# Kernel optimization log

Hardware: AMD Instinct MI355X
Metric: run time of the kernel (lower is better)

The kernel has to match this reference:

```python
import jax, jax.numpy as jnp
import numpy as np

HIDDEN = 2048
N_HEADS = 16
HEAD_DIM = HIDDEN // N_HEADS
FF_DIM = 5632  # int(2*4*2048/3)=5461 rounded up to multiple of 256
ROPE_THETA = 500000.0
NORM_EPS = 1e-5
B, S = 2, 2048


def apply_rope(x, positions, inv_freq):
    # x: [B,S,H,D], positions: [B,S], inv_freq: [D/2]
    angles = positions.astype(inv_freq.dtype)[..., None] * inv_freq[None, None, :]
    cos = jnp.cos(angles)[:, :, None, :]
    sin = jnp.sin(angles)[:, :, None, :]
    x_pair = x.reshape(*x.shape[:-1], x.shape[-1] // 2, 2)
    x0, x1 = x_pair[..., 0], x_pair[..., 1]
    out = jnp.stack([x0 * cos - x1 * sin, x1 * cos + x0 * sin], axis=-1)
    return out.reshape(x.shape).astype(x.dtype)


def rmsnorm(x, scale, eps=NORM_EPS):
    var = jnp.mean(jnp.square(x), axis=-1, keepdims=True)
    return (x * jax.lax.rsqrt(var + eps)) * scale


def setup_inputs() -> dict:
    key = jax.random.key(0)
    ks = jax.random.split(key, 12)
    sd = 1.0 / np.sqrt(HIDDEN)
    sdf = 1.0 / np.sqrt(FF_DIM)
    x = jax.random.normal(ks[0], (B, S, HIDDEN), dtype=jnp.float32)
    positions = jnp.tile(jnp.arange(S, dtype=jnp.int32)[None, :], (B, 1))
    mask = jnp.tril(jnp.ones((S, S), dtype=jnp.bool_))[None].repeat(B, axis=0)
    return {
        "x": x,
        "positions": positions,
        "mask": mask,
        "wq": jax.random.normal(ks[1], (HIDDEN, HIDDEN), jnp.float32) * sd,
        "wk": jax.random.normal(ks[2], (HIDDEN, HIDDEN), jnp.float32) * sd,
        "wv": jax.random.normal(ks[3], (HIDDEN, HIDDEN), jnp.float32) * sd,
        "wo": jax.random.normal(ks[4], (HIDDEN, HIDDEN), jnp.float32) * sd,
        "attn_scale": jnp.ones((HIDDEN,), jnp.float32),
        "ffn_scale": jnp.ones((HIDDEN,), jnp.float32),
        "w1": jax.random.normal(ks[5], (HIDDEN, FF_DIM), jnp.float32) * sd,
        "w3": jax.random.normal(ks[6], (HIDDEN, FF_DIM), jnp.float32) * sd,
        "w2": jax.random.normal(ks[7], (FF_DIM, HIDDEN), jnp.float32) * sdf,
    }


def reference(x, positions, mask, wq, wk, wv, wo, attn_scale, ffn_scale, w1, w3, w2):
    Bx = x.shape[0]
    inv_freq = 1.0 / ROPE_THETA ** (jnp.arange(0, HEAD_DIM, 2, dtype=jnp.float32) / HEAD_DIM)
    x_norm = rmsnorm(x, attn_scale)
    q = apply_rope((x_norm @ wq).reshape(Bx, -1, N_HEADS, HEAD_DIM), positions, inv_freq)
    k = apply_rope((x_norm @ wk).reshape(Bx, -1, N_HEADS, HEAD_DIM), positions, inv_freq)
    v = (x_norm @ wv).reshape(Bx, -1, N_HEADS, HEAD_DIM)
    scale = 1.0 / jnp.sqrt(jnp.float32(HEAD_DIM)).astype(q.dtype)
    # [B,H,S,S]
    attn_weights = jnp.einsum("bqhd,bkhd->bhqk", q, k) * scale
    big_neg = jnp.finfo(q.dtype).min
    attn_weights = jnp.where(mask[:, None, :, :], attn_weights, big_neg)
    attn_weights = jax.nn.softmax(attn_weights, axis=-1)
    attn_out = jnp.einsum("bhqk,bkhd->bqhd", attn_weights, v).reshape(Bx, -1, HIDDEN)
    h = x + attn_out @ wo
    ff = rmsnorm(h, ffn_scale)
    return h + (jax.nn.silu(ff @ w1) * (ff @ w3)) @ w2
```

## Files before the change

kernel.cpp:

```cpp
#include <hip/hip_runtime.h>

#define HID 2048
#define SEQ 2048
#define NB 2
#define NHD 16
#define HD 128
#define FF 5632
#define MROWS 4096

typedef __bf16 bf16x8 __attribute__((ext_vector_type(8)));
typedef float f32x4 __attribute__((ext_vector_type(4)));
typedef unsigned short u16;
typedef unsigned int u32;
typedef unsigned long long u64;

__device__ __forceinline__ u16 f2bf(float f) {
  u32 u = __float_as_uint(f);
  u += 0x7fffu + ((u >> 16) & 1u);
  return (u16)(u >> 16);
}
__device__ __forceinline__ float bf2f(u16 h) {
  return __uint_as_float(((u32)h) << 16);
}
__device__ __forceinline__ void gld16(const void* g, void* l) {
  __builtin_amdgcn_global_load_lds((__attribute__((address_space(1))) void*)g,
                                   (__attribute__((address_space(3))) void*)l, 16, 0, 0);
}

__global__ __launch_bounds__(256) void rmsnorm_k(const float* __restrict__ x,
                                                 const float* __restrict__ sc,
                                                 u16* __restrict__ out) {
  __shared__ float red[4];
  const int row = blockIdx.x, t = threadIdx.x;
  const float4* xr = (const float4*)(x + (size_t)row * HID);
  float4 a = xr[t], b = xr[t + 256];
  float ss = a.x*a.x + a.y*a.y + a.z*a.z + a.w*a.w
           + b.x*b.x + b.y*b.y + b.z*b.z + b.w*b.w;
#pragma unroll
  for (int o = 1; o < 64; o <<= 1) ss += __shfl_xor(ss, o);
  if ((t & 63) == 0) red[t >> 6] = ss;
  __syncthreads();
  float tot = red[0] + red[1] + red[2] + red[3];
  float r = rsqrtf(tot * (1.0f / HID) + 1e-5f);
  const float4* scp = (const float4*)sc;
  float4 s0 = scp[t], s1 = scp[t + 256];
  u32 p0 = (u32)f2bf(a.x*r*s0.x) | ((u32)f2bf(a.y*r*s0.y) << 16);
  u32 p1 = (u32)f2bf(a.z*r*s0.z) | ((u32)f2bf(a.w*r*s0.w) << 16);
  u32 p2 = (u32)f2bf(b.x*r*s1.x) | ((u32)f2bf(b.y*r*s1.y) << 16);
  u32 p3 = (u32)f2bf(b.z*r*s1.z) | ((u32)f2bf(b.w*r*s1.w) << 16);
  u32* op = (u32*)(out + (size_t)row * HID);
  op[t*2] = p0; op[t*2+1] = p1;
  op[512 + t*2] = p2; op[512 + t*2 + 1] = p3;
}

__global__ __launch_bounds__(256) void transpose_cvt_k(const float* __restrict__ W,
                                                       u16* __restrict__ Wt,
                                                       int R, int C) {
  __shared__ float tile[32][33];
  const int tx = threadIdx.x & 31, ty = threadIdx.x >> 5;
  const int bc = blockIdx.x * 32, br = blockIdx.y * 32;
#pragma unroll
  for (int i = 0; i < 4; ++i)
    tile[ty + i*8][tx] = W[(size_t)(br + ty + i*8) * C + bc + tx];
  __syncthreads();
#pragma unroll
  for (int i = 0; i < 4; ++i)
    Wt[(size_t)(bc + ty + i*8) * R + br + tx] = f2bf(tile[tx][ty + i*8]);
}

__global__ __launch_bounds__(256) void rope_k(u16* __restrict__ qk, const int* __restrict__ pos) {
  const u32 i = blockIdx.x * 256 + threadIdx.x;
  const int d2 = i & 63;
  const int s = (i >> 6) & 2047;
  const int bh = i >> 17;
  const int b = bh >> 4;
  const float p = (float)pos[(size_t)b * SEQ + s];
  const float ang = p * exp2f(-(float)d2 * 0.2958057589f);
  float sv, cv;
  sincosf(ang, &sv, &cv);
  u32* ptr = (u32*)(qk + ((size_t)bh * SEQ + s) * HD) + d2;
  u32 u = *ptr;
  float x0 = bf2f((u16)(u & 0xffff)), x1 = bf2f((u16)(u >> 16));
  float o0 = x0 * cv - x1 * sv;
  float o1 = x1 * cv + x0 * sv;
  *ptr = (u32)f2bf(o0) | ((u32)f2bf(o1) << 16);
}

template <int EPI>
__global__ __launch_bounds__(256, 2) void gemm_k(const u16* __restrict__ A,
                                                 const u16* __restrict__ Bt,
                                                 int N, int K,
                                                 const float* addsrc,
                                                 const u16* mulsrc,
                                                 void* outp) {
  __shared__ __align__(16) u16 As[128 * 32];
  __shared__ __align__(16) u16 Bs[128 * 32];
  const int tid = threadIdx.x, lane = tid & 63, wid = tid >> 6;
  const int lr = lane & 15, lg = lane >> 4;
  const int wr = wid >> 1, wc = wid & 1;
  const int mt = blockIdx.y * 128, nt = blockIdx.x * 128;

  const f32x4 fz = {0.f, 0.f, 0.f, 0.f};
  f32x4 acc[4][4];
#pragma unroll
  for (int i = 0; i < 4; ++i)
#pragma unroll
    for (int j = 0; j < 4; ++j) acc[i][j] = fz;

  const int r0 = wid * 32 + (lane >> 2);
  const int c0 = (lane & 3) * 8;
  u16* ldsA0 = As + wid * 1024;
  u16* ldsA1 = As + wid * 1024 + 512;
  u16* ldsB0 = Bs + wid * 1024;
  u16* ldsB1 = Bs + wid * 1024 + 512;
  const u16* Abase = A + (size_t)mt * K;
  const u16* Bbase = Bt + (size_t)nt * K;

  for (int kt = 0; kt < K; kt += 32) {
    gld16(Abase + (size_t)r0 * K + kt + c0, ldsA0);
    gld16(Abase + (size_t)(r0 + 16) * K + kt + c0, ldsA1);
    gld16(Bbase + (size_t)r0 * K + kt + c0, ldsB0);
    gld16(Bbase + (size_t)(r0 + 16) * K + kt + c0, ldsB1);
    __syncthreads();
    bf16x8 af[4], bfr[4];
#pragma unroll
    for (int mi = 0; mi < 4; ++mi)
      af[mi] = *(const bf16x8*)(As + (wr * 64 + mi * 16 + lr) * 32 + lg * 8);
#pragma unroll
    for (int ni = 0; ni < 4; ++ni)
      bfr[ni] = *(const bf16x8*)(Bs + (wc * 64 + ni * 16 + lr) * 32 + lg * 8);
#pragma unroll
    for (int mi = 0; mi < 4; ++mi)
#pragma unroll
      for (int ni = 0; ni < 4; ++ni)
        acc[mi][ni] = __builtin_amdgcn_mfma_f32_16x16x32_bf16(af[mi], bfr[ni], acc[mi][ni], 0, 0, 0);
    __syncthreads();
  }

#pragma unroll
  for (int mi = 0; mi < 4; ++mi) {
#pragma unroll
    for (int ni = 0; ni < 4; ++ni) {
      const int gr0 = mt + wr * 64 + mi * 16 + lg * 4;
      const int gc = nt + wc * 64 + ni * 16 + lr;
      f32x4 v = acc[mi][ni];
      if (EPI == 5) {
        const int b = gr0 >> 11, s = gr0 & 2047, hh = gc >> 7, d = gc & 127;
        u64 pk = (u64)f2bf(v[0])
               | ((u64)f2bf(v[1]) << 16)
               | ((u64)f2bf(v[2]) << 32)
               | ((u64)f2bf(v[3]) << 48);
        *(u64*)((u16*)outp + ((((size_t)(b * NHD + hh)) * HD + d) << 11) + s) = pk;
      } else {
#pragma unroll
        for (int r = 0; r < 4; ++r) {
          const int gr = gr0 + r;
          const float val = v[r];
          if (EPI == 1) {
            const int b = gr >> 11, s = gr & 2047, hh = gc >> 7, d = gc & 127;
            ((u16*)outp)[((((size_t)(b * NHD + hh)) * SEQ + s) << 7) + d] = f2bf(val);
          } else if (EPI == 2) {
            const size_t o = (size_t)gr * N + gc;
            ((float*)outp)[o] = addsrc[o] + val;
          } else if (EPI == 3) {
            const size_t o = (size_t)gr * N + gc;
            ((u16*)outp)[o] = f2bf(val / (1.f + __expf(-val)));
          } else if (EPI == 4) {
            const size_t o = (size_t)gr * N + gc;
            ((u16*)outp)[o] = f2bf(bf2f(mulsrc[o]) * val);
          }
        }
      }
    }
  }
}

#define ATT_SW(row) (((row) & 7) << 4)

__device__ __forceinline__ void att_stage(const u16* __restrict__ Kp,
                                          const u16* __restrict__ Vp,
                                          int kt, char* kb, char* vb,
                                          int tid, int wid) {
#pragma unroll
  for (int j = 0; j < 4; ++j) {
    const int c = j * 256 + tid;
    const int row = c >> 4;
    const int scb = ((c & 15) << 4) ^ ATT_SW(row);
    gld16(Kp + (size_t)(kt + row) * HD + (scb >> 1), kb + j * 4096 + wid * 1024);
  }
#pragma unroll
  for (int j = 0; j < 4; ++j) {
    const int c = j * 256 + tid;
    const int row = c >> 3;
    const int scb = ((c & 7) << 4) ^ ATT_SW(row);
    gld16(Vp + (size_t)row * SEQ + kt + (scb >> 1), vb + j * 4096 + wid * 1024);
  }
}

__global__ __launch_bounds__(256, 2) void attn_k(const u16* __restrict__ Q,
                                                 const u16* __restrict__ Kg,
                                                 const u16* __restrict__ Vtg,
                                                 u16* __restrict__ out) {
  __shared__ __align__(16) char Kb[2][16384];
  __shared__ __align__(16) char Vb[2][16384];
  __shared__ __align__(16) u16 Pl[4][16 * 72];
  const int tid = threadIdx.x, lane = tid & 63, wid = tid >> 6;
  const int lr = lane & 15, lg = lane >> 4;
  int wg = blockIdx.x;
  wg = (wg & 7) * 64 + (wg >> 3);
  const int bh = wg >> 4, pr = wg & 15;
  const size_t bhoff = (size_t)bh * SEQ * HD;
  const u16* Qp = Q + bhoff;
  const u16* Kp = Kg + bhoff;
  const u16* Vp = Vtg + bhoff;
  const int bb = bh >> 4, hh = bh & 15;
  u16* Pw = Pl[wid];
  const int sw = ATT_SW(lr);
  const float scale = 0.08838834764831845f;
  const f32x4 fz = {0.f, 0.f, 0.f, 0.f};

  for (int side = 0; side < 2; ++side) {
    const int qt = side ? (31 - pr) : pr;
    const int qrow0 = qt * 64 + wid * 16;

    bf16x8 qf[4];
#pragma unroll
    for (int t = 0; t < 4; ++t)
      qf[t] = *(const bf16x8*)(Qp + (size_t)(qrow0 + lr) * HD + t * 32 + lg * 8);

    f32x4 o[8];
#pragma unroll
    for (int i = 0; i < 8; ++i) o[i] = fz;
    float mrun[4] = {-1e30f, -1e30f, -1e30f, -1e30f};
    float lrun[4] = {0.f, 0.f, 0.f, 0.f};

    const int kend = qt * 64 + 64;
    int cur = 0;
    att_stage(Kp, Vp, 0, Kb[0], Vb[0], tid, wid);
    __syncthreads();

    for (int kt = 0; kt < kend; kt += 64) {
      if (kt + 64 < kend)
        att_stage(Kp, Vp, kt + 64, Kb[cur ^ 1], Vb[cur ^ 1], tid, wid);
      const char* kbuf = Kb[cur];
      const char* vbuf = Vb[cur];

      f32x4 sc[4];
#pragma unroll
      for (int nh = 0; nh < 4; ++nh) {
        f32x4 s = fz;
#pragma unroll
        for (int t = 0; t < 4; ++t) {
          bf16x8 kf = *(const bf16x8*)(kbuf + (nh * 16 + lr) * 256 + ((t * 64 + lg * 16) ^ sw));
          s = __builtin_amdgcn_mfma_f32_16x16x32_bf16(qf[t], kf, s, 0, 0, 0);
        }
        sc[nh] = s;
      }

      float pv[4][4], alpha[4];
#pragma unroll
      for (int r = 0; r < 4; ++r) {
        const int qrow = qrow0 + lg * 4 + r;
        float s0 = sc[0][r] * scale;
        float s1 = sc[1][r] * scale;
        float s2 = sc[2][r] * scale;
        float s3 = sc[3][r] * scale;
        if (kt + lr > qrow)      s0 = -1e30f;
        if (kt + 16 + lr > qrow) s1 = -1e30f;
        if (kt + 32 + lr > qrow) s2 = -1e30f;
        if (kt + 48 + lr > qrow) s3 = -1e30f;
        float mx = fmaxf(fmaxf(s0, s1), fmaxf(s2, s3));
        mx = fmaxf(mx, __shfl_xor(mx, 1));
        mx = fmaxf(mx, __shfl_xor(mx, 2));
        mx = fmaxf(mx, __shfl_xor(mx, 4));
        mx = fmaxf(mx, __shfl_xor(mx, 8));
        const float mn = fmaxf(mrun[r], mx);
        const float p0 = __expf(s0 - mn), p1 = __expf(s1 - mn);
        const float p2 = __expf(s2 - mn), p3 = __expf(s3 - mn);
        float ts = p0 + p1 + p2 + p3;
        ts += __shfl_xor(ts, 1);
        ts += __shfl_xor(ts, 2);
        ts += __shfl_xor(ts, 4);
        ts += __shfl_xor(ts, 8);
        const float al = __expf(mrun[r] - mn);
        alpha[r] = al;
        lrun[r] = lrun[r] * al + ts;
        mrun[r] = mn;
        pv[0][r] = p0; pv[1][r] = p1; pv[2][r] = p2; pv[3][r] = p3;
      }
#pragma unroll
      for (int i = 0; i < 8; ++i) {
        o[i][0] *= alpha[0]; o[i][1] *= alpha[1];
        o[i][2] *= alpha[2]; o[i][3] *= alpha[3];
      }

#pragma unroll
      for (int nh = 0; nh < 4; ++nh)
#pragma unroll
        for (int r = 0; r < 4; ++r)
          Pw[(lg * 4 + r) * 72 + nh * 16 + lr] = f2bf(pv[nh][r]);
      asm volatile("s_waitcnt lgkmcnt(0)\n" ::: "memory");
      const bf16x8 pf0 = *(const bf16x8*)(Pw + lr * 72 + lg * 8);
      const bf16x8 pf1 = *(const bf16x8*)(Pw + lr * 72 + 32 + lg * 8);

#pragma unroll
      for (int nt = 0; nt < 8; ++nt) {
        const char* vr = vbuf + (nt * 16 + lr) * 128;
        bf16x8 v0 = *(const bf16x8*)(vr + ((lg * 16) ^ sw));
        bf16x8 v1 = *(const bf16x8*)(vr + ((64 + lg * 16) ^ sw));
        o[nt] = __builtin_amdgcn_mfma_f32_16x16x32_bf16(pf0, v0, o[nt], 0, 0, 0);
        o[nt] = __builtin_amdgcn_mfma_f32_16x16x32_bf16(pf1, v1, o[nt], 0, 0, 0);
      }
      __syncthreads();
      cur ^= 1;
    }

#pragma unroll
    for (int r = 0; r < 4; ++r) {
      const int q = qrow0 + lg * 4 + r;
      const float inv = 1.f / lrun[r];
      u16* op = out + ((size_t)(bb * SEQ + q)) * HID + hh * HD + lr;
#pragma unroll
      for (int nt = 0; nt < 8; ++nt)
        op[nt * 16] = f2bf(o[nt][r] * inv);
    }
  }
}

extern "C" void kernel_launch(void* const* d_in, const int* in_sizes, int n_in,
                              void* d_out, int out_size, void* d_ws, size_t ws_size,
                              hipStream_t stream) {
  (void)in_sizes; (void)n_in; (void)out_size; (void)ws_size;
  const float* x   = (const float*)d_in[0];
  const int*   pos = (const int*)d_in[1];
  const float* wq  = (const float*)d_in[3];
  const float* wk  = (const float*)d_in[4];
  const float* wv  = (const float*)d_in[5];
  const float* wo  = (const float*)d_in[6];
  const float* asc = (const float*)d_in[7];
  const float* fsc = (const float*)d_in[8];
  const float* w1  = (const float*)d_in[9];
  const float* w3  = (const float*)d_in[10];
  const float* w2  = (const float*)d_in[11];
  float* out = (float*)d_out;

  char* ws = (char*)d_ws;
  u16* qb = (u16*)ws; ws += (size_t)MROWS * HID * 2;
  u16* kb = (u16*)ws; ws += (size_t)MROWS * HID * 2;
  u16* vb = (u16*)ws; ws += (size_t)MROWS * HID * 2;
  u16* xb = (u16*)ws; ws += (size_t)MROWS * HID * 2;
  u16* gb = (u16*)ws; ws += (size_t)MROWS * FF * 2;
  u16* wb = (u16*)ws; ws += (size_t)FF * HID * 2;

  dim3 b256(256);

  rmsnorm_k<<<MROWS, b256, 0, stream>>>(x, asc, xb);

  transpose_cvt_k<<<dim3(HID/32, HID/32), b256, 0, stream>>>(wq, wb, HID, HID);
  gemm_k<1><<<dim3(HID/128, MROWS/128), b256, 0, stream>>>(xb, wb, HID, HID, nullptr, nullptr, qb);
  transpose_cvt_k<<<dim3(HID/32, HID/32), b256, 0, stream>>>(wk, wb, HID, HID);
  gemm_k<1><<<dim3(HID/128, MROWS/128), b256, 0, stream>>>(xb, wb, HID, HID, nullptr, nullptr, kb);
  transpose_cvt_k<<<dim3(HID/32, HID/32), b256, 0, stream>>>(wv, wb, HID, HID);
  gemm_k<5><<<dim3(HID/128, MROWS/128), b256, 0, stream>>>(xb, wb, HID, HID, nullptr, nullptr, vb);

  rope_k<<<(NB*NHD*SEQ*(HD/2))/256, b256, 0, stream>>>(qb, pos);
  rope_k<<<(NB*NHD*SEQ*(HD/2))/256, b256, 0, stream>>>(kb, pos);

  attn_k<<<dim3(512), b256, 0, stream>>>(qb, kb, vb, xb);

  transpose_cvt_k<<<dim3(HID/32, HID/32), b256, 0, stream>>>(wo, wb, HID, HID);
  gemm_k<2><<<dim3(HID/128, MROWS/128), b256, 0, stream>>>(xb, wb, HID, HID, x, nullptr, out);

  rmsnorm_k<<<MROWS, b256, 0, stream>>>(out, fsc, xb);

  transpose_cvt_k<<<dim3(FF/32, HID/32), b256, 0, stream>>>(w1, wb, HID, FF);
  gemm_k<3><<<dim3(FF/128, MROWS/128), b256, 0, stream>>>(xb, wb, FF, HID, nullptr, nullptr, gb);
  transpose_cvt_k<<<dim3(FF/32, HID/32), b256, 0, stream>>>(w3, wb, HID, FF);
  gemm_k<4><<<dim3(FF/128, MROWS/128), b256, 0, stream>>>(xb, wb, FF, HID, nullptr, gb, gb);
  transpose_cvt_k<<<dim3(HID/32, FF/32), b256, 0, stream>>>(w2, wb, FF, HID);
  gemm_k<2><<<dim3(HID/128, MROWS/128), b256, 0, stream>>>(gb, wb, HID, FF, out, nullptr, out);
}
```

Measured before the change: 1.003 ms.

## Replace GEMM with 256x256 double-buffered pipelined kernel and fuse QKV projection

```diff
diff --git a/kernel.cpp b/kernel.cpp
--- a/kernel.cpp
+++ b/kernel.cpp
@@ -86,80 +86,139 @@
   *ptr = (u32)f2bf(o0) | ((u32)f2bf(o1) << 16);
 }
 
+#define VMW(N) asm volatile("s_waitcnt vmcnt(" #N ")" ::: "memory")
+#define BARR() do { __builtin_amdgcn_s_barrier(); __builtin_amdgcn_sched_barrier(0); } while (0)
+
+#define STAGE_A(NB, H) do { \
+  gld16(ap + (size_t)((H)*128) * K,      &Ab[NB][(H)*8192 + wid*512]); \
+  gld16(ap + (size_t)((H)*128 + 64) * K, &Ab[NB][(H)*8192 + 4096 + wid*512]); \
+} while (0)
+#define STAGE_B(NB, H) do { \
+  gld16(bp + (size_t)((H)*128) * K,      &Bb[NB][(H)*8192 + wid*512]); \
+  gld16(bp + (size_t)((H)*128 + 64) * K, &Bb[NB][(H)*8192 + 4096 + wid*512]); \
+} while (0)
+#define READ_A(BF, AH) do { \
+  const char* pa_ = (const char*)Ab[BF] + (AH)*16384 + arow; \
+  av[0][0] = *(const bf16x8*)(pa_ + 0*4096 + ck0); av[0][1] = *(const bf16x8*)(pa_ + 0*4096 + ck1); \
+  av[1][0] = *(const bf16x8*)(pa_ + 1*4096 + ck0); av[1][1] = *(const bf16x8*)(pa_ + 1*4096 + ck1); \
+  av[2][0] = *(const bf16x8*)(pa_ + 2*4096 + ck0); av[2][1] = *(const bf16x8*)(pa_ + 2*4096 + ck1); \
+  av[3][0] = *(const bf16x8*)(pa_ + 3*4096 + ck0); av[3][1] = *(const bf16x8*)(pa_ + 3*4096 + ck1); \
+} while (0)
+#define READ_B(BF, BH) do { \
+  const char* pb_ = (const char*)Bb[BF] + (BH)*16384 + brow; \
+  bv[(BH)*2+0][0] = *(const bf16x8*)(pb_ + 0*8192 + ck0); bv[(BH)*2+0][1] = *(const bf16x8*)(pb_ + 0*8192 + ck1); \
+  bv[(BH)*2+1][0] = *(const bf16x8*)(pb_ + 1*8192 + ck0); bv[(BH)*2+1][1] = *(const bf16x8*)(pb_ + 1*8192 + ck1); \
+} while (0)
+#define MMAQ(AH, BH) do { \
+  __builtin_amdgcn_s_setprio(1); \
+  _Pragma("unroll") \
+  for (int kk_ = 0; kk_ < 2; ++kk_) \
+    _Pragma("unroll") \
+    for (int m_ = 0; m_ < 4; ++m_) \
+      _Pragma("unroll") \
+      for (int n_ = 0; n_ < 2; ++n_) \
+        acc[(AH)*4+m_][(BH)*2+n_] = __builtin_amdgcn_mfma_f32_16x16x32_bf16( \
+            av[m_][kk_], bv[(BH)*2+n_][kk_], acc[(AH)*4+m_][(BH)*2+n_], 0, 0, 0); \
+  __builtin_amdgcn_s_setprio(0); \
+} while (0)
+
 template <int EPI>
-__global__ __launch_bounds__(256, 2) void gemm_k(const u16* __restrict__ A,
-                                                 const u16* __restrict__ Bt,
-                                                 int N, int K,
-                                                 const float* addsrc,
-                                                 const u16* mulsrc,
-                                                 void* outp) {
-  __shared__ __align__(16) u16 As[128 * 32];
-  __shared__ __align__(16) u16 Bs[128 * 32];
+__global__ __launch_bounds__(512, 2) void gemm256_k(const u16* __restrict__ A,
+                                                    const u16* __restrict__ Bt,
+                                                    int N, int K,
+                                                    const float* __restrict__ addsrc,
+                                                    const u16* __restrict__ mulsrc,
+                                                    void* __restrict__ outp) {
+  __shared__ __align__(16) u16 Ab[2][16384];
+  __shared__ __align__(16) u16 Bb[2][16384];
   const int tid = threadIdx.x, lane = tid & 63, wid = tid >> 6;
   const int lr = lane & 15, lg = lane >> 4;
-  const int wr = wid >> 1, wc = wid & 1;
-  const int mt = blockIdx.y * 128, nt = blockIdx.x * 128;
+  const int wr = wid >> 2, wc = wid & 3;
+
+  const int gx = gridDim.x;
+  int bid = blockIdx.y * gx + blockIdx.x;
+  const int q8 = (gx * gridDim.y) >> 3;
+  bid = (bid & 7) * q8 + (bid >> 3);
+  const int mt = (bid / gx) * 256, nt = (bid % gx) * 256;
 
   const f32x4 fz = {0.f, 0.f, 0.f, 0.f};
-  f32x4 acc[4][4];
-#pragma unroll
-  for (int i = 0; i < 4; ++i)
+  f32x4 acc[8][4];
+#pragma unroll
+  for (int i = 0; i < 8; ++i)
 #pragma unroll
     for (int j = 0; j < 4; ++j) acc[i][j] = fz;
 
-  const int r0 = wid * 32 + (lane >> 2);
-  const int c0 = (lane & 3) * 8;
-  u16* ldsA0 = As + wid * 1024;
-  u16* ldsA1 = As + wid * 1024 + 512;
-  u16* ldsB0 = Bs + wid * 1024;
-  u16* ldsB1 = Bs + wid * 1024 + 512;
-  const u16* Abase = A + (size_t)mt * K;
-  const u16* Bbase = Bt + (size_t)nt * K;
-
-  for (int kt = 0; kt < K; kt += 32) {
-    gld16(Abase + (size_t)r0 * K + kt + c0, ldsA0);
-    gld16(Abase + (size_t)(r0 + 16) * K + kt + c0, ldsA1);
-    gld16(Bbase + (size_t)r0 * K + kt + c0, ldsB0);
-    gld16(Bbase + (size_t)(r0 + 16) * K + kt + c0, ldsB1);
-    __syncthreads();
-    bf16x8 af[4], bfr[4];
-#pragma unroll
-    for (int mi = 0; mi < 4; ++mi)
-      af[mi] = *(const bf16x8*)(As + (wr * 64 + mi * 16 + lr) * 32 + lg * 8);
-#pragma unroll
-    for (int ni = 0; ni < 4; ++ni)
-      bfr[ni] = *(const bf16x8*)(Bs + (wc * 64 + ni * 16 + lr) * 32 + lg * 8);
-#pragma unroll
-    for (int mi = 0; mi < 4; ++mi)
-#pragma unroll
-      for (int ni = 0; ni < 4; ++ni)
-        acc[mi][ni] = __builtin_amdgcn_mfma_f32_16x16x32_bf16(af[mi], bfr[ni], acc[mi][ni], 0, 0, 0);
-    __syncthreads();
+  const int srow = tid >> 3;
+  const int scol = ((((tid & 7) * 16) ^ (((srow >> 2) & 1) << 5)) >> 1);
+  const u16* ap = A  + (size_t)(mt + srow) * K + scol;
+  const u16* bp = Bt + (size_t)(nt + srow) * K + scol;
+
+  const int arow = (wr * 16 + lr) * 128;
+  const int brow = (wc * 16 + lr) * 128;
+  const int swl = ((lr >> 2) & 1) << 5;
+  const int ck0 = (lg * 16) ^ swl;
+  const int ck1 = (64 + lg * 16) ^ swl;
+
+  bf16x8 av[4][2], bv[4][2];
+
+  STAGE_A(0, 0); STAGE_B(0, 0); STAGE_B(0, 1); STAGE_A(0, 1);
+  ap += 64; bp += 64;
+
+  const int ntk = K >> 6;
+  int buf = 0;
+  for (int t = 0; t < ntk - 1; ++t) {
+    const int nb = buf ^ 1;
+    STAGE_A(nb, 0);  VMW(6); BARR();
+    READ_A(buf, 0);  READ_B(buf, 0);  MMAQ(0, 0);
+    STAGE_B(nb, 0);  VMW(6); BARR();
+    READ_B(buf, 1);  MMAQ(0, 1);
+    STAGE_B(nb, 1);  VMW(6); BARR();
+    READ_A(buf, 1);  MMAQ(1, 1);
+    STAGE_A(nb, 1);
+    MMAQ(1, 0);
+    ap += 64; bp += 64;
+    buf = nb;
   }
-
-#pragma unroll
-  for (int mi = 0; mi < 4; ++mi) {
+  VMW(4); BARR();
+  READ_A(buf, 0); READ_B(buf, 0); MMAQ(0, 0);
+  VMW(2); BARR();
+  READ_B(buf, 1); MMAQ(0, 1);
+  VMW(0); BARR();
+  READ_A(buf, 1); MMAQ(1, 1);
+  MMAQ(1, 0);
+
+#pragma unroll
+  for (int mi = 0; mi < 8; ++mi) {
 #pragma unroll
     for (int ni = 0; ni < 4; ++ni) {
-      const int gr0 = mt + wr * 64 + mi * 16 + lg * 4;
-      const int gc = nt + wc * 64 + ni * 16 + lr;
+      const int gr0 = mt + mi * 32 + wr * 16 + lg * 4;
+      const int gc = nt + ni * 64 + wc * 16 + lr;
       f32x4 v = acc[mi][ni];
-      if (EPI == 5) {
-        const int b = gr0 >> 11, s = gr0 & 2047, hh = gc >> 7, d = gc & 127;
-        u64 pk = (u64)f2bf(v[0])
-               | ((u64)f2bf(v[1]) << 16)
-               | ((u64)f2bf(v[2]) << 32)
-               | ((u64)f2bf(v[3]) << 48);
-        *(u64*)((u16*)outp + ((((size_t)(b * NHD + hh)) * HD + d) << 11) + s) = pk;
+      if (EPI == 1) {
+        const int which = gc >> 11;
+        const int c2 = gc & 2047;
+        const int hh = c2 >> 7, d = c2 & 127;
+        if (which < 2) {
+          u16* dst = (u16*)outp + (size_t)which * ((size_t)MROWS * HID);
+#pragma unroll
+          for (int r = 0; r < 4; ++r) {
+            const int gr = gr0 + r;
+            const int b = gr >> 11, s = gr & 2047;
+            dst[((((size_t)(b * NHD + hh)) * SEQ + s) << 7) + d] = f2bf(v[r]);
+          }
+        } else {
+          u16* dst = (u16*)outp + (size_t)2 * ((size_t)MROWS * HID);
+          const int b = gr0 >> 11, s0 = gr0 & 2047;
+          u64 pk = (u64)f2bf(v[0]) | ((u64)f2bf(v[1]) << 16)
+                 | ((u64)f2bf(v[2]) << 32) | ((u64)f2bf(v[3]) << 48);
+          *(u64*)(dst + ((((size_t)(b * NHD + hh)) * HD + d) << 11) + s0) = pk;
+        }
       } else {
 #pragma unroll
         for (int r = 0; r < 4; ++r) {
           const int gr = gr0 + r;
           const float val = v[r];
-          if (EPI == 1) {
-            const int b = gr >> 11, s = gr & 2047, hh = gc >> 7, d = gc & 127;
-            ((u16*)outp)[((((size_t)(b * NHD + hh)) * SEQ + s) << 7) + d] = f2bf(val);
-          } else if (EPI == 2) {
+          if (EPI == 2) {
             const size_t o = (size_t)gr * N + gc;
             ((float*)outp)[o] = addsrc[o] + val;
           } else if (EPI == 3) {
@@ -245,7 +304,7 @@
       const char* kbuf = Kb[cur];
       const char* vbuf = Vb[cur];
 
-      f32x4 sc[4];
+      f32x4 sc2[4];
 #pragma unroll
       for (int nh = 0; nh < 4; ++nh) {
         f32x4 s = fz;
@@ -254,17 +313,17 @@
           bf16x8 kf = *(const bf16x8*)(kbuf + (nh * 16 + lr) * 256 + ((t * 64 + lg * 16) ^ sw));
           s = __builtin_amdgcn_mfma_f32_16x16x32_bf16(qf[t], kf, s, 0, 0, 0);
         }
-        sc[nh] = s;
+        sc2[nh] = s;
       }
 
       float pv[4][4], alpha[4];
 #pragma unroll
       for (int r = 0; r < 4; ++r) {
         const int qrow = qrow0 + lg * 4 + r;
-        float s0 = sc[0][r] * scale;
-        float s1 = sc[1][r] * scale;
-        float s2 = sc[2][r] * scale;
-        float s3 = sc[3][r] * scale;
+        float s0 = sc2[0][r] * scale;
+        float s1 = sc2[1][r] * scale;
+        float s2 = sc2[2][r] * scale;
+        float s3 = sc2[3][r] * scale;
         if (kt + lr > qrow)      s0 = -1e30f;
         if (kt + 16 + lr > qrow) s1 = -1e30f;
         if (kt + 32 + lr > qrow) s2 = -1e30f;
@@ -304,12 +363,12 @@
       const bf16x8 pf1 = *(const bf16x8*)(Pw + lr * 72 + 32 + lg * 8);
 
 #pragma unroll
-      for (int nt = 0; nt < 8; ++nt) {
-        const char* vr = vbuf + (nt * 16 + lr) * 128;
+      for (int nt2 = 0; nt2 < 8; ++nt2) {
+        const char* vr = vbuf + (nt2 * 16 + lr) * 128;
         bf16x8 v0 = *(const bf16x8*)(vr + ((lg * 16) ^ sw));
         bf16x8 v1 = *(const bf16x8*)(vr + ((64 + lg * 16) ^ sw));
-        o[nt] = __builtin_amdgcn_mfma_f32_16x16x32_bf16(pf0, v0, o[nt], 0, 0, 0);
-        o[nt] = __builtin_amdgcn_mfma_f32_16x16x32_bf16(pf1, v1, o[nt], 0, 0, 0);
+        o[nt2] = __builtin_amdgcn_mfma_f32_16x16x32_bf16(pf0, v0, o[nt2], 0, 0, 0);
+        o[nt2] = __builtin_amdgcn_mfma_f32_16x16x32_bf16(pf1, v1, o[nt2], 0, 0, 0);
       }
       __syncthreads();
       cur ^= 1;
@@ -321,8 +380,8 @@
       const float inv = 1.f / lrun[r];
       u16* op = out + ((size_t)(bb * SEQ + q)) * HID + hh * HD + lr;
 #pragma unroll
-      for (int nt = 0; nt < 8; ++nt)
-        op[nt * 16] = f2bf(o[nt][r] * inv);
+      for (int nt2 = 0; nt2 < 8; ++nt2)
+        op[nt2 * 16] = f2bf(o[nt2][r] * inv);
     }
   }
 }
@@ -351,17 +410,16 @@
   u16* xb = (u16*)ws; ws += (size_t)MROWS * HID * 2;
   u16* gb = (u16*)ws; ws += (size_t)MROWS * FF * 2;
   u16* wb = (u16*)ws; ws += (size_t)FF * HID * 2;
-
-  dim3 b256(256);
+  u16* wqkvT = gb;
+
+  dim3 b256(256), b512(512);
 
   rmsnorm_k<<<MROWS, b256, 0, stream>>>(x, asc, xb);
 
-  transpose_cvt_k<<<dim3(HID/32, HID/32), b256, 0, stream>>>(wq, wb, HID, HID);
-  gemm_k<1><<<dim3(HID/128, MROWS/128), b256, 0, stream>>>(xb, wb, HID, HID, nullptr, nullptr, qb);
-  transpose_cvt_k<<<dim3(HID/32, HID/32), b256, 0, stream>>>(wk, wb, HID, HID);
-  gemm_k<1><<<dim3(HID/128, MROWS/128), b256, 0, stream>>>(xb, wb, HID, HID, nullptr, nullptr, kb);
-  transpose_cvt_k<<<dim3(HID/32, HID/32), b256, 0, stream>>>(wv, wb, HID, HID);
-  gemm_k<5><<<dim3(HID/128, MROWS/128), b256, 0, stream>>>(xb, wb, HID, HID, nullptr, nullptr, vb);
+  transpose_cvt_k<<<dim3(HID/32, HID/32), b256, 0, stream>>>(wq, wqkvT, HID, HID);
+  transpose_cvt_k<<<dim3(HID/32, HID/32), b256, 0, stream>>>(wk, wqkvT + (size_t)HID*HID, HID, HID);
+  transpose_cvt_k<<<dim3(HID/32, HID/32), b256, 0, stream>>>(wv, wqkvT + (size_t)2*HID*HID, HID, HID);
+  gemm256_k<1><<<dim3(3*HID/256, MROWS/256), b512, 0, stream>>>(xb, wqkvT, 3*HID, HID, nullptr, nullptr, qb);
 
   rope_k<<<(NB*NHD*SEQ*(HD/2))/256, b256, 0, stream>>>(qb, pos);
   rope_k<<<(NB*NHD*SEQ*(HD/2))/256, b256, 0, stream>>>(kb, pos);
@@ -369,14 +427,14 @@
   attn_k<<<dim3(512), b256, 0, stream>>>(qb, kb, vb, xb);
 
   transpose_cvt_k<<<dim3(HID/32, HID/32), b256, 0, stream>>>(wo, wb, HID, HID);
-  gemm_k<2><<<dim3(HID/128, MROWS/128), b256, 0, stream>>>(xb, wb, HID, HID, x, nullptr, out);
+  gemm256_k<2><<<dim3(HID/256, MROWS/256), b512, 0, stream>>>(xb, wb, HID, HID, x, nullptr, out);
 
   rmsnorm_k<<<MROWS, b256, 0, stream>>>(out, fsc, xb);
 
   transpose_cvt_k<<<dim3(FF/32, HID/32), b256, 0, stream>>>(w1, wb, HID, FF);
-  gemm_k<3><<<dim3(FF/128, MROWS/128), b256, 0, stream>>>(xb, wb, FF, HID, nullptr, nullptr, gb);
+  gemm256_k<3><<<dim3(FF/256, MROWS/256), b512, 0, stream>>>(xb, wb, FF, HID, nullptr, nullptr, gb);
   transpose_cvt_k<<<dim3(FF/32, HID/32), b256, 0, stream>>>(w3, wb, HID, FF);
-  gemm_k<4><<<dim3(FF/128, MROWS/128), b256, 0, stream>>>(xb, wb, FF, HID, nullptr, gb, gb);
+  gemm256_k<4><<<dim3(FF/256, MROWS/256), b512, 0, stream>>>(xb, wb, FF, HID, nullptr, gb, gb);
   transpose_cvt_k<<<dim3(HID/32, FF/32), b256, 0, stream>>>(w2, wb, FF, HID);
-  gemm_k<2><<<dim3(HID/128, MROWS/128), b256, 0, stream>>>(gb, wb, HID, FF, out, nullptr, out);
-}
+  gemm256_k<2><<<dim3(HID/256, MROWS/256), b512, 0, stream>>>(gb, wb, HID, FF, out, nullptr, out);
+}
```

Measured after the change: 1.016 ms. No clear change (+1.3%).
